# Kernel tuning notes

Measured on AMD Instinct MI355X. Metric: run time of the kernel, lower is better.

## Reference

```python
import jax, jax.numpy as jnp
import numpy as np

SCALE_H, SCALE_W = 160.0, 160.0  # init spatial_scale
ALIGNED = False


def setup_inputs() -> dict:
    key = jax.random.key(0)
    k1, k2, k3 = jax.random.split(key, 3)
    feats = jax.random.normal(k1, (4, 256, 160, 160), dtype=jnp.float32)
    B, N = 4, 512
    bidx = jax.random.randint(k2, (N,), 0, B).astype(jnp.float32)
    p = jax.random.uniform(k3, (N, 4), dtype=jnp.float32)
    x1 = p[:, 0] * 0.7
    y1 = p[:, 1] * 0.7
    x2 = x1 + 0.05 + p[:, 2] * 0.25
    y2 = y1 + 0.05 + p[:, 3] * 0.25
    rois = jnp.stack([bidx, x1, y1, x2, y2], axis=1)
    return {
        "input_images_or_features": feats,
        "rois": rois,
        "output_height": 14,
        "output_width": 14,
    }


def reference(input_images_or_features, rois, output_height, output_width):
    feats = input_images_or_features  # [B, C, H, W]
    B, C, H, W = feats.shape
    OH, OW = int(output_height), int(output_width)
    dt = rois.dtype

    b = rois[:, 0].astype(jnp.int32)                      # [N]
    x1 = rois[:, 1] * SCALE_W
    y1 = rois[:, 2] * SCALE_H
    x2 = rois[:, 3] * SCALE_W
    y2 = rois[:, 4] * SCALE_H
    rw = x2 - x1
    rh = y2 - y1

    xs = jnp.arange(OW, dtype=dt) / max(OW - 1, 1)
    ys = jnp.arange(OH, dtype=dt) / max(OH - 1, 1)
    gy, gx = jnp.meshgrid(ys, xs, indexing="ij")          # [OH, OW]

    fx = x1[:, None, None] + gx[None] * rw[:, None, None]  # [N, OH, OW]
    fy = y1[:, None, None] + gy[None] * rh[:, None, None]

    if ALIGNED:
        nfx = fx / (W - 1) * 2 - 1
        nfy = fy / (H - 1) * 2 - 1
        ix = (nfx + 1) / 2 * (W - 1)
        iy = (nfy + 1) / 2 * (H - 1)
    else:
        nfx = fx / W * 2 - 1
        nfy = fy / H * 2 - 1
        ix = ((nfx + 1) * W - 1) / 2
        iy = ((nfy + 1) * H - 1) / 2

    x0f = jnp.floor(ix)
    y0f = jnp.floor(iy)
    x0 = x0f.astype(jnp.int32)
    y0 = y0f.astype(jnp.int32)

    wx1 = ix - x0f   # weight for x0+1
    wx0 = 1.0 - wx1
    wy1 = iy - y0f
    wy0 = 1.0 - wy1

    bb = b[:, None, None]

    def corner(yi, xi, w):
        valid = (xi >= 0) & (xi < W) & (yi >= 0) & (yi < H)
        xc = jnp.clip(xi, 0, W - 1)
        yc = jnp.clip(yi, 0, H - 1)
        v = feats[bb, :, yc, xc]                 # [N, OH, OW, C]
        return v * (w * valid.astype(dt))[..., None]

    out = (corner(y0, x0, wy0 * wx0)
           + corner(y0, x0 + 1, wy0 * wx1)
           + corner(y0 + 1, x0, wy1 * wx0)
           + corner(y0 + 1, x0 + 1, wy1 * wx1))   # [N, OH, OW, C]
    return jnp.transpose(out, (0, 3, 1, 2))       # [N, C, OH, OW]
```

## Files before the change

### kernel.cpp

```cpp
#include <hip/hip_runtime.h>
#include <cstddef>
#include <cstdint>

#define RA_C   256
#define RA_H   160
#define RA_W   160
#define RA_OH  14
#define RA_OW  14
#define RA_S   196
#define RA_SCALE 160.0f

#define CQ     32
#define NCQ    (RA_C / CQ)
#define NBIN   (4 * RA_H)
#define MAXE   128
#define CHUNK  48
#define ROW_F  164
#define CH_F   332

struct XParam { int p; float w0, w1; };

__device__ __forceinline__ XParam axis_param(float lo, float ext, int o,
                                             float inv, int lim)
{
    float g   = (float)o * inv;
    float f   = lo + g * ext;
    float nf  = f / (float)lim * 2.0f - 1.0f;
    float ix  = ((nf + 1.0f) * (float)lim - 1.0f) * 0.5f;
    float i0f = floorf(ix);
    int   i0  = (int)i0f;
    float w1  = ix - i0f, w0 = 1.0f - w1;
    bool  v0  = (i0 >= 0) && (i0 < lim);
    int   ip  = i0 + 1;
    bool  v1  = (ip >= 0) && (ip < lim);
    float W0  = w0 * (v0 ? 1.0f : 0.0f);
    float W1  = w1 * (v1 ? 1.0f : 0.0f);
    int   p   = min(max(i0, 0), lim - 2);
    bool  swp = (i0 != p);
    XParam r;
    r.p  = p;
    r.w0 = swp ? W1 : W0;
    r.w1 = swp ? W0 : W1;
    return r;
}

__global__ __launch_bounds__(256) void roi_prep_kernel(
    const float* __restrict__ rois,
    float4* __restrict__ xq,
    int2*   __restrict__ xp,
    float2* __restrict__ yw,
    int* __restrict__ counts, unsigned short* __restrict__ entries, int N)
{
    int t = blockIdx.x * 256 + (int)threadIdx.x;
    if (t >= N * RA_OH) return;
    int n = t / RA_OH, i = t - n * RA_OH;
    const float* r = rois + (size_t)n * 5;
    int   b  = (int)r[0];
    float x1 = r[1] * RA_SCALE;
    float y1 = r[2] * RA_SCALE;
    float rw = r[3] * RA_SCALE - x1;
    float rh = r[4] * RA_SCALE - y1;

    XParam yp = axis_param(y1, rh, i, 1.0f / (RA_OH - 1), RA_H);
    yw[t] = make_float2(yp.w0, yp.w1);
    int bin = b * RA_H + yp.p;
    int pos = atomicAdd(&counts[bin], 1);
    if (pos < MAXE)
        entries[(size_t)bin * MAXE + pos] = (unsigned short)((n << 4) | i);

    if (i < RA_OW / 2) {
        XParam xa = axis_param(x1, rw, 2 * i,     1.0f / (RA_OW - 1), RA_W);
        XParam xb = axis_param(x1, rw, 2 * i + 1, 1.0f / (RA_OW - 1), RA_W);
        xq[n * 7 + i] = make_float4(xa.w0, xa.w1, xb.w0, xb.w1);
        xp[n * 7 + i] = make_int2(xa.p, xb.p);
    }
}

__global__ __launch_bounds__(256) void roi_main_kernel(
    const float* __restrict__ feats, float* __restrict__ out,
    const float4* __restrict__ xq, const int2* __restrict__ xp,
    const float2* __restrict__ yw,
    const int* __restrict__ counts, const unsigned short* __restrict__ entries)
{
    __shared__ __align__(16) float win[CQ * CH_F];
    __shared__ int    s_ent[CHUNK];
    __shared__ float2 s_wy[CHUNK];
    __shared__ __align__(16) float4 s_xw[CHUNK][7];
    __shared__ int2   s_xi[CHUNK][7];

    constexpr int HW = RA_H * RA_W;

    int bid = blockIdx.x;
    int cq  = bid & (NCQ - 1);
    int bin = bid >> 3;
    int cnt = counts[bin];
    if (cnt == 0) return;
    if (cnt > MAXE) cnt = MAXE;
    int b = bin / RA_H;
    int p = bin - b * RA_H;
    int tid = (int)threadIdx.x;
    int c0 = cq * CQ;

    const float* fb = feats + (((size_t)b * RA_C + c0) * RA_H + p) * RA_W;
    for (int i = tid; i < CQ * 2 * (RA_W / 4); i += 256) {
        int c   = i / 80;
        int rem = i - c * 80;
        int row = rem / 40;
        int x4  = rem - row * 40;
        float4 v = *(const float4*)(fb + (size_t)c * HW + row * RA_W + x4 * 4);
        *(float4*)&win[c * CH_F + row * ROW_F + x4 * 4] = v;
    }

    int c  = tid / 7;
    int j  = tid - c * 7;
    bool act = tid < CQ * 7;
    int oofs = (c0 + c) * RA_S + 2 * j;
    const unsigned short* el = entries + (size_t)bin * MAXE;
    const float* wc = &win[c * CH_F];

    for (int base = 0; base < cnt; base += CHUNK) {
        int m = min(CHUNK, cnt - base);

        if (base) __syncthreads();
        if (tid < m) {
            int ent = el[base + tid];
            s_ent[tid] = ent;
            s_wy[tid]  = yw[(ent >> 4) * RA_OH + (ent & 15)];
        }
        __syncthreads();

        for (int i = tid; i < m * 7; i += 256) {
            int e = i / 7, jj = i - e * 7;
            int n = s_ent[e] >> 4;
            s_xw[e][jj] = xq[n * 7 + jj];
            s_xi[e][jj] = xp[n * 7 + jj];
        }
        __syncthreads();

        for (int e = 0; e < m; ++e) {
            int ent = __builtin_amdgcn_readfirstlane(s_ent[e]);
            int n = ent >> 4, oy = ent & 15;
            float2 wy = s_wy[e];
            if (act) {
                float4 xw = s_xw[e][j];
                int2   xi = s_xi[e][j];
                const float* pa = wc + xi.x;
                const float* pb = wc + xi.y;
                float p00 = pa[0],     p01 = pa[1];
                float p10 = pa[ROW_F], p11 = pa[ROW_F + 1];
                float q00 = pb[0],     q01 = pb[1];
                float q10 = pb[ROW_F], q11 = pb[ROW_F + 1];

                float a0 = wy.x * xw.x, b0 = wy.x * xw.y;
                float a1 = wy.y * xw.x, b1 = wy.y * xw.y;
                float v0 = fmaf(a0, p00, fmaf(b0, p01, fmaf(a1, p10, b1 * p11)));
                float c0w = wy.x * xw.z, d0 = wy.x * xw.w;
                float c1w = wy.y * xw.z, d1 = wy.y * xw.w;
                float v1 = fmaf(c0w, q00, fmaf(d0, q01, fmaf(c1w, q10, d1 * q11)));

                float* ob = out + ((size_t)n * RA_C * RA_S + oy * RA_OW + oofs);
                *(float2*)ob = make_float2(v0, v1);
            }
        }
    }
}

__device__ __forceinline__ float2 ldg_f2(const float* p) {
    float2 r;
    __builtin_memcpy(&r, p, sizeof(float2));
    return r;
}

__global__ __launch_bounds__(256) void roi_align_fallback(
    const float* __restrict__ feats, const float* __restrict__ rois,
    float* __restrict__ out, int N, int bpc)
{
    constexpr int S   = RA_OH * RA_OW;
    constexpr int K   = 8;
    constexpr int CG  = RA_C / K;
    constexpr int CGX = CG / 8;
    constexpr int HW  = RA_H * RA_W;

    int bid   = blockIdx.x;
    int xcd   = bid & 7;
    int local = bid >> 3;
    int cg    = xcd * CGX + local / bpc;
    int rem   = local - (local / bpc) * bpc;
    int idx_in_cg = rem * 256 + (int)threadIdx.x;
    if (idx_in_cg >= N * S) return;
    int n = idx_in_cg / S;
    int s = idx_in_cg - n * S;
    int oy = s / RA_OW;
    int ox = s - oy * RA_OW;

    const float* r = rois + (size_t)n * 5;
    int   b  = (int)r[0];
    float x1 = r[1] * RA_SCALE;
    float y1 = r[2] * RA_SCALE;
    float rw = r[3] * RA_SCALE - x1;
    float rh = r[4] * RA_SCALE - y1;
    XParam xpr = axis_param(x1, rw, ox, 1.0f / (RA_OW - 1), RA_W);
    XParam ypr = axis_param(y1, rh, oy, 1.0f / (RA_OH - 1), RA_H);
    float a0 = ypr.w0 * xpr.w0, b0 = ypr.w0 * xpr.w1;
    float a1 = ypr.w1 * xpr.w0, b1 = ypr.w1 * xpr.w1;
    int o0 = ypr.p * RA_W + xpr.p;
    int o1 = o0 + RA_W;

    int c0 = cg * K;
    const float* fbp = feats + ((size_t)b * RA_C + c0) * HW;
    float*       op  = out   + ((size_t)n * RA_C + c0) * S + s;
#pragma unroll
    for (int k = 0; k < K; ++k) {
        const float* f = fbp + (size_t)k * HW;
        float2 p0 = ldg_f2(f + o0);
        float2 p1 = ldg_f2(f + o1);
        float v = fmaf(a0, p0.x, fmaf(b0, p0.y, fmaf(a1, p1.x, b1 * p1.y)));
        op[(size_t)k * S] = v;
    }
}

extern "C" void kernel_launch(void* const* d_in, const int* in_sizes, int n_in,
                              void* d_out, int out_size, void* d_ws, size_t ws_size,
                              hipStream_t stream) {
    const float* feats = (const float*)d_in[0];
    const float* rois  = (const float*)d_in[1];
    float*       out   = (float*)d_out;

    int N = in_sizes[1] / 5;

    size_t off_xp  = (size_t)N * 7 * 16;
    size_t off_yw  = off_xp + (size_t)N * 7 * 8;
    size_t off_cnt = off_yw + (size_t)N * 14 * 8;
    size_t off_ent = off_cnt + (size_t)NBIN * 4;
    size_t need    = off_ent + (size_t)NBIN * MAXE * 2;

    if (d_ws != nullptr && ws_size >= need && N <= 512) {
        char* ws = (char*)d_ws;
        float4* xq = (float4*)ws;
        int2*   xp = (int2*)(ws + off_xp);
        float2* yw = (float2*)(ws + off_yw);
        int*    counts = (int*)(ws + off_cnt);
        unsigned short* entries = (unsigned short*)(ws + off_ent);

        hipMemsetAsync(counts, 0, NBIN * sizeof(int), stream);
        int gridA = (N * RA_OH + 255) / 256;
        roi_prep_kernel<<<gridA, 256, 0, stream>>>(rois, xq, xp, yw,
                                                   counts, entries, N);
        roi_main_kernel<<<NBIN * NCQ, 256, 0, stream>>>(feats, out, xq, xp, yw,
                                                        counts, entries);
    } else {
        constexpr int S = RA_OH * RA_OW;
        int bpc  = (N * S + 255) / 256;
        int grid = (RA_C / 8) * bpc;
        roi_align_fallback<<<grid, 256, 0, stream>>>(feats, rois, out, N, bpc);
    }
}
```

Before: 239.7 us.

## Halve channel slice per block and process two entries per iteration

Reduces channels per block from 32 to 16, doubling the grid, and splits the 256 threads into two halves that each handle a different ROI row entry per loop step. Previously only 224 of 256 threads were active. Now 224 of 256 threads work on two entries at once, halving the serial entry loop. The per-entry x-parameter loads are folded into the single staging step, removing one barrier, but that step is now serialized over 7 iterations in a few threads. The feature window is loaded once per channel half, so global window reads stay the same while block count doubles.

```diff
diff --git a/kernel.cpp b/kernel.cpp
--- a/kernel.cpp
+++ b/kernel.cpp
@@ -10,7 +10,7 @@
 #define RA_S   196
 #define RA_SCALE 160.0f
 
-#define CQ     32
+#define CQ     16
 #define NCQ    (RA_C / CQ)
 #define NBIN   (4 * RA_H)
 #define MAXE   128
@@ -92,7 +92,7 @@
 
     int bid = blockIdx.x;
     int cq  = bid & (NCQ - 1);
-    int bin = bid >> 3;
+    int bin = bid >> 4;
     int cnt = counts[bin];
     if (cnt == 0) return;
     if (cnt > MAXE) cnt = MAXE;
@@ -111,9 +111,11 @@
         *(float4*)&win[c * CH_F + row * ROW_F + x4 * 4] = v;
     }
 
-    int c  = tid / 7;
-    int j  = tid - c * 7;
-    bool act = tid < CQ * 7;
+    int half = tid & 127;
+    int par  = tid >> 7;
+    int c  = half / 7;
+    int j  = half - c * 7;
+    bool geo = half < CQ * 7;
     int oofs = (c0 + c) * RA_S + 2 * j;
     const unsigned short* el = entries + (size_t)bin * MAXE;
     const float* wc = &win[c * CH_F];
@@ -125,25 +127,25 @@
         if (tid < m) {
             int ent = el[base + tid];
             s_ent[tid] = ent;
-            s_wy[tid]  = yw[(ent >> 4) * RA_OH + (ent & 15)];
+            int n = ent >> 4;
+            s_wy[tid] = yw[n * RA_OH + (ent & 15)];
+#pragma unroll
+            for (int jj = 0; jj < 7; ++jj) {
+                s_xw[tid][jj] = xq[n * 7 + jj];
+                s_xi[tid][jj] = xp[n * 7 + jj];
+            }
         }
         __syncthreads();
 
-        for (int i = tid; i < m * 7; i += 256) {
-            int e = i / 7, jj = i - e * 7;
-            int n = s_ent[e] >> 4;
-            s_xw[e][jj] = xq[n * 7 + jj];
-            s_xi[e][jj] = xp[n * 7 + jj];
-        }
-        __syncthreads();
-
-        for (int e = 0; e < m; ++e) {
-            int ent = __builtin_amdgcn_readfirstlane(s_ent[e]);
+        for (int e = 0; e < m; e += 2) {
+            int idx = e + par;
+            bool act = geo && (idx < m);
+            int ent = __builtin_amdgcn_readfirstlane(s_ent[idx]);
             int n = ent >> 4, oy = ent & 15;
-            float2 wy = s_wy[e];
+            float2 wy = s_wy[idx];
             if (act) {
-                float4 xw = s_xw[e][j];
-                int2   xi = s_xi[e][j];
+                float4 xw = s_xw[idx][j];
+                int2   xi = s_xi[idx][j];
                 const float* pa = wc + xi.x;
                 const float* pb = wc + xi.y;
                 float p00 = pa[0],     p01 = pa[1];
```

After: 219.4 us. 8.4% less time.
